# Kernel tuning notes

Measured on AMD Instinct MI355X. Metric: run time of the kernel, lower is better.

## Reference

```python
import jax, jax.numpy as jnp
import numpy as np

SIGMA_S = 10.0
SIGMA_R = 0.5
NUM_ITER = 3
EPS = 1e-8


def _gauss_kernel(sigma_s):
    # static python (sigma_s is config), matches torch code exactly
    ks = min(int(6 * sigma_s + 1), 61)
    if ks % 2 == 0:
        ks -= 1
    hk = ks // 2
    x = jnp.arange(-hk, hk + 1, dtype=jnp.float32)
    g = jnp.exp(-(x ** 2) / (2.0 * sigma_s ** 2))
    return g / g.sum(), hk


def _depthwise_1d(img, g, hk, axis):
    """Depthwise Gaussian conv along axis (2=H, 3=W) with replicate padding.
    img: [B,C,H,W]. Equivalent to the original unfold+gaussian reduction."""
    C = img.shape[1]
    ks = g.shape[0]
    pad = [(0, 0)] * 4
    pad[axis] = (hk, hk)
    p = jnp.pad(img, pad, mode='edge')
    if axis == 3:
        rhs = jnp.broadcast_to(g.reshape(1, 1, 1, ks), (C, 1, 1, ks))
    else:
        rhs = jnp.broadcast_to(g.reshape(1, 1, ks, 1), (C, 1, ks, 1))
    return jax.lax.conv_general_dilated(
        p, rhs, window_strides=(1, 1), padding='VALID',
        dimension_numbers=('NCHW', 'OIHW', 'NCHW'),
        feature_group_count=C)


def _edge_weights(guide, sigma_r):
    # grad along W, replicate last column; grad along H, replicate last row
    gx = guide[:, :, :, 1:] - guide[:, :, :, :-1]
    gx = jnp.pad(gx, ((0, 0), (0, 0), (0, 0), (0, 1)), mode='edge')
    gy = guide[:, :, 1:, :] - guide[:, :, :-1, :]
    gy = jnp.pad(gy, ((0, 0), (0, 0), (0, 1), (0, 0)), mode='edge')
    inv2s2 = 1.0 / (2.0 * sigma_r ** 2)
    wx = jnp.exp(-(gx ** 2) * inv2s2)
    wy = jnp.exp(-(gy ** 2) * inv2s2)
    return wx, wy


def _dt_filter(input_img):
    # guide = channel mean (C>1 branch of the original)
    guide = input_img.mean(axis=1, keepdims=True)  # [B,1,H,W]
    wx, wy = _edge_weights(guide, SIGMA_R)
    # NOTE: in the original, weight = gauss_k * w(x); weight_sum = w(x)*sum(gauss)+eps
    # = w(x)+eps (gauss is normalized). Since w(x) is constant over k, the weighted
    # reduction factorizes exactly: out = (w/(w+eps)) * gaussian_conv(img).
    # Same math, no [B,C,H,W,K] unfold tensor.
    sx = wx / (wx + EPS)  # scale used by vertical filter
    sy = wy / (wy + EPS)  # scale used by horizontal filter
    out = input_img
    for i in range(NUM_ITER):
        sigma_i = SIGMA_S * 2 ** i
        g, hk = _gauss_kernel(sigma_i)
        out = _depthwise_1d(out, g, hk, axis=3) * sy  # horizontal, vert-grad weights
        out = _depthwise_1d(out, g, hk, axis=2) * sx  # vertical, horiz-grad weights
    return out  # mode='denoise': no detail enhancement


def setup_inputs() -> dict:
    key = jax.random.key(0)
    input_img = jax.random.uniform(key, (8, 3, 1024, 1024), dtype=jnp.float32)
    return {"input_img": input_img}


def reference(input_img):
    return _dt_filter(input_img)
```

## Files before the change

kernel.cpp:

```cpp
#include <hip/hip_runtime.h>
#include <math.h>


#define HH 1024
#define WW 1024
#define BB 8
#define CC 3
#define KS 61
#define HK 30

struct GW { float w[KS]; };

__global__ __launch_bounds__(512) void hconv(const float* __restrict__ in,
                                             float* __restrict__ out, GW g) {
    __shared__ float tile[64][193];
    const int xt  = blockIdx.x;
    const int yt  = blockIdx.y;
    const int bc  = blockIdx.z;
    const int tid = threadIdx.x;

    const float* src   = in + (size_t)bc * (HH * (size_t)WW);
    const int    xbase = xt * 128 - 32;
    const int    y0    = yt * 64;

    {
        const int rg = tid >> 6, lane = tid & 63;
        #pragma unroll
        for (int k = 0; k < 8; ++k) {
            const int r = rg + 8 * k;
            const float* srow = src + (size_t)(y0 + r) * WW;
            #pragma unroll
            for (int m = 0; m < 3; ++m) {
                const int c = lane + 64 * m;
                int gx = xbase + c;
                gx = min(max(gx, 0), WW - 1);
                tile[r][c] = srow[gx];
            }
        }
    }
    __syncthreads();

    const int y  = tid & 63;
    const int xg = tid >> 6;
    const int cb = xg * 16 + 2;

    float acc[16];
    #pragma unroll
    for (int i = 0; i < 16; ++i) acc[i] = 0.f;

    #pragma unroll
    for (int j = 0; j < 16 + KS - 1; ++j) {
        const float v = tile[y][cb + j];
        #pragma unroll
        for (int i = 0; i < 16; ++i) {
            const int t = j - i;
            if (t >= 0 && t < KS)
                acc[i] = fmaf(g.w[t], v, acc[i]);
        }
    }

    float* dst = out + (size_t)bc * (HH * (size_t)WW)
                     + (size_t)(y0 + y) * WW + xt * 128 + xg * 16;
    #pragma unroll
    for (int i = 0; i < 4; ++i)
        *(float4*)(dst + 4 * i) = make_float4(acc[4*i], acc[4*i+1],
                                              acc[4*i+2], acc[4*i+3]);
}

__global__ __launch_bounds__(512) void vconv(const float* __restrict__ in,
                                             float* __restrict__ out, GW g) {
    __shared__ float tile[(128 + 2 * HK) * 64];
    const int bx0 = blockIdx.x * 64;
    const int ty0 = blockIdx.y * 128;
    const int bc  = blockIdx.z;
    const int tid = threadIdx.x;

    const float* src = in + (size_t)bc * (HH * (size_t)WW);

    {
        const int rg = tid >> 5, lane = tid & 31;
        #pragma unroll
        for (int k = 0; k < 12; ++k) {
            const int r = rg + 16 * k;
            if (r < 188) {
                int gy = ty0 + r - HK;
                gy = min(max(gy, 0), HH - 1);
                const float2* srow = (const float2*)(src + (size_t)gy * WW + bx0);
                ((float2*)tile)[r * 32 + lane] = srow[lane];
            }
        }
    }
    __syncthreads();

    const int x  = tid & 63;
    const int yg = tid >> 6;
    const int yo = yg * 16;

    float acc[16];
    #pragma unroll
    for (int i = 0; i < 16; ++i) acc[i] = 0.f;

    #pragma unroll
    for (int j = 0; j < 16 + KS - 1; ++j) {
        const float v = tile[(yo + j) * 64 + x];
        #pragma unroll
        for (int i = 0; i < 16; ++i) {
            const int t = j - i;
            if (t >= 0 && t < KS)
                acc[i] = fmaf(g.w[t], v, acc[i]);
        }
    }

    float* dst = out + (size_t)bc * (HH * (size_t)WW)
                     + (size_t)(ty0 + yo) * WW + bx0 + x;
    #pragma unroll
    for (int i = 0; i < 16; ++i) dst[(size_t)i * WW] = acc[i];
}

static void fill_w(double sigma, GW* g) {
    double tmp[KS], s = 0.0;
    for (int k = 0; k < KS; ++k) {
        const double d = (double)(k - HK);
        tmp[k] = exp(-(d * d) / (2.0 * sigma * sigma));
        s += tmp[k];
    }
    for (int k = 0; k < KS; ++k) g->w[k] = (float)(tmp[k] / s);
}

extern "C" void kernel_launch(void* const* d_in, const int* in_sizes, int n_in,
                              void* d_out, int out_size, void* d_ws, size_t ws_size,
                              hipStream_t stream) {
    const float* input = (const float*)d_in[0];
    float* out = (float*)d_out;
    float* tmp = (float*)d_ws;

    GW g10, g20, g40;
    fill_w(10.0, &g10);
    fill_w(20.0, &g20);
    fill_w(40.0, &g40);

    const dim3 hb(512), hg(WW / 128, HH / 64, BB * CC);
    const dim3 vb(512), vg(WW / 64, HH / 128, BB * CC);

    hconv<<<hg, hb, 0, stream>>>(input, tmp, g10);
    vconv<<<vg, vb, 0, stream>>>(tmp, out, g10);
    hconv<<<hg, hb, 0, stream>>>(out, tmp, g20);
    vconv<<<vg, vb, 0, stream>>>(tmp, out, g20);
    hconv<<<hg, hb, 0, stream>>>(out, tmp, g40);
    vconv<<<vg, vb, 0, stream>>>(tmp, out, g40);
}
```

Baseline: 451.9 us.

## Drop shared-memory tiles and register-block 32 outputs per thread in both convolutions

Both the horizontal and vertical Gaussian passes stop staging a tile in LDS and instead read inputs straight from global memory. The horizontal pass uses float4 row loads, with clamping only at image edges. Each thread now accumulates 32 outputs in registers instead of 16, which cuts the halo overhead per output, and the grids are reshaped to match. This removes LDS traffic and the block barrier, in exchange for relying on the L1/L2 caches for overlapping window reads and for higher register pressure, which may lower occupancy.

```diff
diff --git a/kernel.cpp b/kernel.cpp
--- a/kernel.cpp
+++ b/kernel.cpp
@@ -11,110 +11,83 @@
 
 struct GW { float w[KS]; };
 
-__global__ __launch_bounds__(512) void hconv(const float* __restrict__ in,
+__global__ __launch_bounds__(256) void hconv(const float* __restrict__ in,
                                              float* __restrict__ out, GW g) {
-    __shared__ float tile[64][193];
-    const int xt  = blockIdx.x;
-    const int yt  = blockIdx.y;
+    const int tid = threadIdx.x;
+    const int seg = tid & 31;
+    const int row = tid >> 5;
+    const int y   = blockIdx.x * 8 + row;
     const int bc  = blockIdx.z;
-    const int tid = threadIdx.x;
 
-    const float* src   = in + (size_t)bc * (HH * (size_t)WW);
-    const int    xbase = xt * 128 - 32;
-    const int    y0    = yt * 64;
+    const float* __restrict__ srow = in + ((size_t)bc * HH + y) * WW;
+    const int X  = seg * 32;
+    const int xw = X - 32;
 
-    {
-        const int rg = tid >> 6, lane = tid & 63;
+    float acc[32];
+    #pragma unroll
+    for (int i = 0; i < 32; ++i) acc[i] = 0.f;
+
+    #pragma unroll
+    for (int k = 0; k < 24; ++k) {
+        const int gx = xw + 4 * k;
+        float4 v;
+        if (gx >= 0 && gx <= WW - 4) {
+            v = *(const float4*)(srow + gx);
+        } else {
+            const int a0 = min(max(gx    , 0), WW - 1);
+            const int a1 = min(max(gx + 1, 0), WW - 1);
+            const int a2 = min(max(gx + 2, 0), WW - 1);
+            const int a3 = min(max(gx + 3, 0), WW - 1);
+            v = make_float4(srow[a0], srow[a1], srow[a2], srow[a3]);
+        }
+        const float vv[4] = { v.x, v.y, v.z, v.w };
         #pragma unroll
-        for (int k = 0; k < 8; ++k) {
-            const int r = rg + 8 * k;
-            const float* srow = src + (size_t)(y0 + r) * WW;
+        for (int c = 0; c < 4; ++c) {
+            const int j = 4 * k + c;
             #pragma unroll
-            for (int m = 0; m < 3; ++m) {
-                const int c = lane + 64 * m;
-                int gx = xbase + c;
-                gx = min(max(gx, 0), WW - 1);
-                tile[r][c] = srow[gx];
+            for (int i = 0; i < 32; ++i) {
+                const int t = j - 2 - i;
+                if (t >= 0 && t < KS)
+                    acc[i] = fmaf(g.w[t], vv[c], acc[i]);
             }
         }
     }
-    __syncthreads();
 
-    const int y  = tid & 63;
-    const int xg = tid >> 6;
-    const int cb = xg * 16 + 2;
+    float* drow = out + ((size_t)bc * HH + y) * WW + X;
+    #pragma unroll
+    for (int i = 0; i < 8; ++i)
+        *(float4*)(drow + 4 * i) =
+            make_float4(acc[4*i], acc[4*i+1], acc[4*i+2], acc[4*i+3]);
+}
 
-    float acc[16];
+__global__ __launch_bounds__(256) void vconv(const float* __restrict__ in,
+                                             float* __restrict__ out, GW g) {
+    const int x  = blockIdx.x * 256 + threadIdx.x;
+    const int Y  = blockIdx.y * 32;
+    const int bc = blockIdx.z;
+
+    const float* __restrict__ src = in + (size_t)bc * (HH * (size_t)WW);
+
+    float acc[32];
     #pragma unroll
-    for (int i = 0; i < 16; ++i) acc[i] = 0.f;
+    for (int i = 0; i < 32; ++i) acc[i] = 0.f;
 
     #pragma unroll
-    for (int j = 0; j < 16 + KS - 1; ++j) {
-        const float v = tile[y][cb + j];
+    for (int j = 0; j < 32 + KS - 1; ++j) {
+        int gy = Y - HK + j;
+        gy = min(max(gy, 0), HH - 1);
+        const float v = src[(size_t)gy * WW + x];
         #pragma unroll
-        for (int i = 0; i < 16; ++i) {
+        for (int i = 0; i < 32; ++i) {
             const int t = j - i;
             if (t >= 0 && t < KS)
                 acc[i] = fmaf(g.w[t], v, acc[i]);
         }
     }
 
-    float* dst = out + (size_t)bc * (HH * (size_t)WW)
-                     + (size_t)(y0 + y) * WW + xt * 128 + xg * 16;
+    float* dst = out + (size_t)bc * (HH * (size_t)WW) + (size_t)Y * WW + x;
     #pragma unroll
-    for (int i = 0; i < 4; ++i)
-        *(float4*)(dst + 4 * i) = make_float4(acc[4*i], acc[4*i+1],
-                                              acc[4*i+2], acc[4*i+3]);
-}
-
-__global__ __launch_bounds__(512) void vconv(const float* __restrict__ in,
-                                             float* __restrict__ out, GW g) {
-    __shared__ float tile[(128 + 2 * HK) * 64];
-    const int bx0 = blockIdx.x * 64;
-    const int ty0 = blockIdx.y * 128;
-    const int bc  = blockIdx.z;
-    const int tid = threadIdx.x;
-
-    const float* src = in + (size_t)bc * (HH * (size_t)WW);
-
-    {
-        const int rg = tid >> 5, lane = tid & 31;
-        #pragma unroll
-        for (int k = 0; k < 12; ++k) {
-            const int r = rg + 16 * k;
-            if (r < 188) {
-                int gy = ty0 + r - HK;
-                gy = min(max(gy, 0), HH - 1);
-                const float2* srow = (const float2*)(src + (size_t)gy * WW + bx0);
-                ((float2*)tile)[r * 32 + lane] = srow[lane];
-            }
-        }
-    }
-    __syncthreads();
-
-    const int x  = tid & 63;
-    const int yg = tid >> 6;
-    const int yo = yg * 16;
-
-    float acc[16];
-    #pragma unroll
-    for (int i = 0; i < 16; ++i) acc[i] = 0.f;
-
-    #pragma unroll
-    for (int j = 0; j < 16 + KS - 1; ++j) {
-        const float v = tile[(yo + j) * 64 + x];
-        #pragma unroll
-        for (int i = 0; i < 16; ++i) {
-            const int t = j - i;
-            if (t >= 0 && t < KS)
-                acc[i] = fmaf(g.w[t], v, acc[i]);
-        }
-    }
-
-    float* dst = out + (size_t)bc * (HH * (size_t)WW)
-                     + (size_t)(ty0 + yo) * WW + bx0 + x;
-    #pragma unroll
-    for (int i = 0; i < 16; ++i) dst[(size_t)i * WW] = acc[i];
+    for (int i = 0; i < 32; ++i) dst[(size_t)i * WW] = acc[i];
 }
 
 static void fill_w(double sigma, GW* g) {
@@ -139,8 +112,8 @@
     fill_w(20.0, &g20);
     fill_w(40.0, &g40);
 
-    const dim3 hb(512), hg(WW / 128, HH / 64, BB * CC);
-    const dim3 vb(512), vg(WW / 64, HH / 128, BB * CC);
+    const dim3 hb(256), hg(HH / 8, 1, BB * CC);
+    const dim3 vb(256), vg(WW / 256, HH / 32, BB * CC);
 
     hconv<<<hg, hb, 0, stream>>>(input, tmp, g10);
     vconv<<<vg, vb, 0, stream>>>(tmp, out, g10);
```

Measured after the change: 1.555 ms. 244% more time.

## Compose three Gaussian passes into one 181-tap filter with separate edge kernels

Applied to the files above, without the earlier changes.

Precomputes, on the host, the convolution of the sigma 10, 20 and 40 Gaussians into a single 181-tap kernel. Interior pixels are then filtered with one horizontal and one vertical pass instead of three of each. The border bands, where replicate padding breaks that composition, get dedicated kernels that chain the three 61-tap passes inside shared memory. This cuts global memory round trips and launches, at the cost of larger shared tiles, lower occupancy from 256-thread blocks, and extra edge launches.

```diff
diff --git a/kernel.cpp b/kernel.cpp
--- a/kernel.cpp
+++ b/kernel.cpp
@@ -6,125 +6,290 @@
 #define WW 1024
 #define BB 8
 #define CC 3
-#define KS 61
-#define HK 30
-
-struct GW { float w[KS]; };
-
-__global__ __launch_bounds__(512) void hconv(const float* __restrict__ in,
-                                             float* __restrict__ out, GW g) {
-    __shared__ float tile[64][193];
-    const int xt  = blockIdx.x;
-    const int yt  = blockIdx.y;
-    const int bc  = blockIdx.z;
-    const int tid = threadIdx.x;
-
-    const float* src   = in + (size_t)bc * (HH * (size_t)WW);
-    const int    xbase = xt * 128 - 32;
-    const int    y0    = yt * 64;
-
+
+struct GW181 { float w[181]; };
+struct GW3   { float a[61]; float b[61]; float c[61]; };
+
+__global__ __launch_bounds__(256) void hfused(const float* __restrict__ in,
+                                              float* __restrict__ out, GW181 g) {
+    __shared__ float tile[32][309];
+    const int x0 = 90 + 128 * blockIdx.x;
+    const int y0 = blockIdx.y * 32;
+    const int bc = blockIdx.z;
+    const int t  = threadIdx.x;
+
+    const float* __restrict__ src = in + ((size_t)bc * HH + y0) * WW;
     {
-        const int rg = tid >> 6, lane = tid & 63;
+        const int lane = t & 63, rg = t >> 6;
         #pragma unroll
         for (int k = 0; k < 8; ++k) {
+            const int r = rg + 4 * k;
+            const float* srow = src + (size_t)r * WW;
+            #pragma unroll
+            for (int m = 0; m < 5; ++m) {
+                const int c = lane + 64 * m;
+                if (c < 308) tile[r][c] = srow[min(x0 - 90 + c, WW - 1)];
+            }
+        }
+    }
+    __syncthreads();
+
+    const int y = t & 31, xg = t >> 5;
+    float acc[16];
+    #pragma unroll
+    for (int i = 0; i < 16; ++i) acc[i] = 0.f;
+
+    #pragma unroll
+    for (int j = 0; j < 196; ++j) {
+        const float v = tile[y][xg * 16 + j];
+        #pragma unroll
+        for (int i = 0; i < 16; ++i) {
+            const int tt = j - i;
+            if (tt >= 0 && tt < 181) acc[i] = fmaf(g.w[tt], v, acc[i]);
+        }
+    }
+
+    float* drow = out + ((size_t)bc * HH + y0 + y) * WW + x0 + xg * 16;
+    #pragma unroll
+    for (int i = 0; i < 16; ++i)
+        if (x0 + xg * 16 + i < 934) drow[i] = acc[i];
+}
+
+__global__ __launch_bounds__(256) void vfused(const float* __restrict__ in,
+                                              float* __restrict__ out, GW181 g) {
+    __shared__ float tile[308][32];
+    const int Y0 = 90 + 128 * blockIdx.x;
+    const int x0 = blockIdx.y * 32;
+    const int bc = blockIdx.z;
+    const int t  = threadIdx.x;
+
+    const float* __restrict__ src = in + (size_t)bc * (HH * (size_t)WW);
+    {
+        const int col = t & 31, rg = t >> 5;
+        #pragma unroll
+        for (int k = 0; k < 39; ++k) {
             const int r = rg + 8 * k;
-            const float* srow = src + (size_t)(y0 + r) * WW;
-            #pragma unroll
-            for (int m = 0; m < 3; ++m) {
+            if (r < 308) {
+                const int u = min(Y0 - 90 + r, HH - 1);
+                tile[r][col] = src[(size_t)u * WW + x0 + col];
+            }
+        }
+    }
+    __syncthreads();
+
+    const int col = t & 31, yo = (t >> 5) * 16;
+    float acc[16];
+    #pragma unroll
+    for (int i = 0; i < 16; ++i) acc[i] = 0.f;
+
+    #pragma unroll
+    for (int j = 0; j < 196; ++j) {
+        const float v = tile[yo + j][col];
+        #pragma unroll
+        for (int i = 0; i < 16; ++i) {
+            const int tt = j - i;
+            if (tt >= 0 && tt < 181) acc[i] = fmaf(g.w[tt], v, acc[i]);
+        }
+    }
+
+    float* dst = out + (size_t)bc * (HH * (size_t)WW) + x0 + col;
+    #pragma unroll
+    for (int i = 0; i < 16; ++i) {
+        const int yy = Y0 + yo + i;
+        if (yy < 934) dst[(size_t)yy * WW] = acc[i];
+    }
+}
+
+__global__ __launch_bounds__(256) void hedge(const float* __restrict__ in,
+                                             float* __restrict__ out, GW3 g) {
+    __shared__ float s0[16][217], s1[16][185], s2[16][153];
+    const int ys   = blockIdx.x;
+    const int bc   = blockIdx.y;
+    const int side = blockIdx.z;
+    const int t    = threadIdx.x;
+
+    const float* __restrict__ src = in + ((size_t)bc * HH + ys * 16) * WW;
+    {
+        const int lane = t & 63, rg = t >> 6;
+        #pragma unroll
+        for (int k = 0; k < 4; ++k) {
+            const int r = rg + 4 * k;
+            #pragma unroll
+            for (int m = 0; m < 4; ++m) {
                 const int c = lane + 64 * m;
-                int gx = xbase + c;
-                gx = min(max(gx, 0), WW - 1);
-                tile[r][c] = srow[gx];
-            }
-        }
-    }
-    __syncthreads();
-
-    const int y  = tid & 63;
-    const int xg = tid >> 6;
-    const int cb = xg * 16 + 2;
-
-    float acc[16];
-    #pragma unroll
-    for (int i = 0; i < 16; ++i) acc[i] = 0.f;
-
-    #pragma unroll
-    for (int j = 0; j < 16 + KS - 1; ++j) {
-        const float v = tile[y][cb + j];
-        #pragma unroll
-        for (int i = 0; i < 16; ++i) {
-            const int t = j - i;
-            if (t >= 0 && t < KS)
-                acc[i] = fmaf(g.w[t], v, acc[i]);
-        }
-    }
-
-    float* dst = out + (size_t)bc * (HH * (size_t)WW)
-                     + (size_t)(y0 + y) * WW + xt * 128 + xg * 16;
-    #pragma unroll
-    for (int i = 0; i < 4; ++i)
-        *(float4*)(dst + 4 * i) = make_float4(acc[4*i], acc[4*i+1],
-                                              acc[4*i+2], acc[4*i+3]);
-}
-
-__global__ __launch_bounds__(512) void vconv(const float* __restrict__ in,
-                                             float* __restrict__ out, GW g) {
-    __shared__ float tile[(128 + 2 * HK) * 64];
-    const int bx0 = blockIdx.x * 64;
-    const int ty0 = blockIdx.y * 128;
-    const int bc  = blockIdx.z;
-    const int tid = threadIdx.x;
-
-    const float* src = in + (size_t)bc * (HH * (size_t)WW);
-
+                if (c < 217) {
+                    int u = max(c - 32, 0);
+                    if (side) u = WW - 1 - u;
+                    s0[r][c] = src[(size_t)r * WW + u];
+                }
+            }
+        }
+    }
+    __syncthreads();
+
+    const int y = t >> 4, xl = t & 15;
+
+    if (xl < 15) {
+        float a[10];
+        #pragma unroll
+        for (int i = 0; i < 10; ++i) a[i] = 0.f;
+        const int z0 = 10 * xl;
+        #pragma unroll
+        for (int j = 0; j < 70; ++j) {
+            const float v = s0[y][z0 + 2 + j];
+            #pragma unroll
+            for (int i = 0; i < 10; ++i) {
+                const int r = j - i;
+                if (r >= 0 && r < 61) a[i] = fmaf(g.a[r], v, a[i]);
+            }
+        }
+        #pragma unroll
+        for (int i = 0; i < 10; ++i) s1[y][z0 + 32 + i] = a[i];
+        if (xl == 0)
+            for (int p = 0; p < 32; ++p) s1[y][p] = a[0];
+    }
+    __syncthreads();
+
+    if (xl < 15) {
+        float a[8];
+        #pragma unroll
+        for (int i = 0; i < 8; ++i) a[i] = 0.f;
+        const int z0 = 8 * xl;
+        #pragma unroll
+        for (int j = 0; j < 68; ++j) {
+            const float v = s1[y][z0 + 2 + j];
+            #pragma unroll
+            for (int i = 0; i < 8; ++i) {
+                const int r = j - i;
+                if (r >= 0 && r < 61) a[i] = fmaf(g.b[r], v, a[i]);
+            }
+        }
+        #pragma unroll
+        for (int i = 0; i < 8; ++i) s2[y][z0 + 32 + i] = a[i];
+        if (xl == 0)
+            for (int p = 0; p < 32; ++p) s2[y][p] = a[0];
+    }
+    __syncthreads();
+
+    if (xl < 15) {
+        float a[6];
+        #pragma unroll
+        for (int i = 0; i < 6; ++i) a[i] = 0.f;
+        const int z0 = 6 * xl;
+        #pragma unroll
+        for (int j = 0; j < 66; ++j) {
+            const float v = s2[y][z0 + 2 + j];
+            #pragma unroll
+            for (int i = 0; i < 6; ++i) {
+                const int r = j - i;
+                if (r >= 0 && r < 61) a[i] = fmaf(g.c[r], v, a[i]);
+            }
+        }
+        float* drow = out + ((size_t)bc * HH + ys * 16 + y) * WW;
+        #pragma unroll
+        for (int i = 0; i < 6; ++i) {
+            const int gx = z0 + i;
+            drow[side ? (WW - 1 - gx) : gx] = a[i];
+        }
+    }
+}
+
+__global__ __launch_bounds__(256) void vedge(const float* __restrict__ in,
+                                             float* __restrict__ out, GW3 g) {
+    __shared__ float s0[217][17], s1[185][17], s2[153][17];
+    const int xs   = blockIdx.x;
+    const int bc   = blockIdx.y;
+    const int side = blockIdx.z;
+    const int t    = threadIdx.x;
+    const int cx   = t & 15, zl = t >> 4;
+
+    const float* __restrict__ src = in + (size_t)bc * (HH * (size_t)WW);
     {
-        const int rg = tid >> 5, lane = tid & 31;
-        #pragma unroll
-        for (int k = 0; k < 12; ++k) {
-            const int r = rg + 16 * k;
-            if (r < 188) {
-                int gy = ty0 + r - HK;
-                gy = min(max(gy, 0), HH - 1);
-                const float2* srow = (const float2*)(src + (size_t)gy * WW + bx0);
-                ((float2*)tile)[r * 32 + lane] = srow[lane];
-            }
-        }
-    }
-    __syncthreads();
-
-    const int x  = tid & 63;
-    const int yg = tid >> 6;
-    const int yo = yg * 16;
-
-    float acc[16];
-    #pragma unroll
-    for (int i = 0; i < 16; ++i) acc[i] = 0.f;
-
-    #pragma unroll
-    for (int j = 0; j < 16 + KS - 1; ++j) {
-        const float v = tile[(yo + j) * 64 + x];
-        #pragma unroll
-        for (int i = 0; i < 16; ++i) {
-            const int t = j - i;
-            if (t >= 0 && t < KS)
-                acc[i] = fmaf(g.w[t], v, acc[i]);
-        }
-    }
-
-    float* dst = out + (size_t)bc * (HH * (size_t)WW)
-                     + (size_t)(ty0 + yo) * WW + bx0 + x;
-    #pragma unroll
-    for (int i = 0; i < 16; ++i) dst[(size_t)i * WW] = acc[i];
-}
-
-static void fill_w(double sigma, GW* g) {
-    double tmp[KS], s = 0.0;
-    for (int k = 0; k < KS; ++k) {
-        const double d = (double)(k - HK);
-        tmp[k] = exp(-(d * d) / (2.0 * sigma * sigma));
-        s += tmp[k];
-    }
-    for (int k = 0; k < KS; ++k) g->w[k] = (float)(tmp[k] / s);
+        #pragma unroll
+        for (int k = 0; k < 14; ++k) {
+            const int r = zl + 16 * k;
+            if (r < 217) {
+                int u = max(r - 32, 0);
+                if (side) u = HH - 1 - u;
+                s0[r][cx] = src[(size_t)u * WW + xs * 16 + cx];
+            }
+        }
+    }
+    __syncthreads();
+
+    if (zl < 15) {
+        float a[10];
+        #pragma unroll
+        for (int i = 0; i < 10; ++i) a[i] = 0.f;
+        const int z0 = 10 * zl;
+        #pragma unroll
+        for (int j = 0; j < 70; ++j) {
+            const float v = s0[z0 + 2 + j][cx];
+            #pragma unroll
+            for (int i = 0; i < 10; ++i) {
+                const int r = j - i;
+                if (r >= 0 && r < 61) a[i] = fmaf(g.a[r], v, a[i]);
+            }
+        }
+        #pragma unroll
+        for (int i = 0; i < 10; ++i) s1[z0 + 32 + i][cx] = a[i];
+        if (zl == 0)
+            for (int p = 0; p < 32; ++p) s1[p][cx] = a[0];
+    }
+    __syncthreads();
+
+    if (zl < 15) {
+        float a[8];
+        #pragma unroll
+        for (int i = 0; i < 8; ++i) a[i] = 0.f;
+        const int z0 = 8 * zl;
+        #pragma unroll
+        for (int j = 0; j < 68; ++j) {
+            const float v = s1[z0 + 2 + j][cx];
+            #pragma unroll
+            for (int i = 0; i < 8; ++i) {
+                const int r = j - i;
+                if (r >= 0 && r < 61) a[i] = fmaf(g.b[r], v, a[i]);
+            }
+        }
+        #pragma unroll
+        for (int i = 0; i < 8; ++i) s2[z0 + 32 + i][cx] = a[i];
+        if (zl == 0)
+            for (int p = 0; p < 32; ++p) s2[p][cx] = a[0];
+    }
+    __syncthreads();
+
+    if (zl < 15) {
+        float a[6];
+        #pragma unroll
+        for (int i = 0; i < 6; ++i) a[i] = 0.f;
+        const int z0 = 6 * zl;
+        #pragma unroll
+        for (int j = 0; j < 66; ++j) {
+            const float v = s2[z0 + 2 + j][cx];
+            #pragma unroll
+            for (int i = 0; i < 6; ++i) {
+                const int r = j - i;
+                if (r >= 0 && r < 61) a[i] = fmaf(g.c[r], v, a[i]);
+            }
+        }
+        #pragma unroll
+        for (int i = 0; i < 6; ++i) {
+            const int gy = z0 + i;
+            const int Y  = side ? (HH - 1 - gy) : gy;
+            out[(size_t)bc * (HH * (size_t)WW) + (size_t)Y * WW + xs * 16 + cx] = a[i];
+        }
+    }
+}
+
+static void gauss61(double sigma, double* w) {
+    double s = 0.0;
+    for (int k = 0; k < 61; ++k) {
+        const double d = (double)(k - 30);
+        w[k] = exp(-(d * d) / (2.0 * sigma * sigma));
+        s += w[k];
+    }
+    for (int k = 0; k < 61; ++k) w[k] /= s;
 }
 
 extern "C" void kernel_launch(void* const* d_in, const int* in_sizes, int n_in,
@@ -134,18 +299,32 @@
     float* out = (float*)d_out;
     float* tmp = (float*)d_ws;
 
-    GW g10, g20, g40;
-    fill_w(10.0, &g10);
-    fill_w(20.0, &g20);
-    fill_w(40.0, &g40);
-
-    const dim3 hb(512), hg(WW / 128, HH / 64, BB * CC);
-    const dim3 vb(512), vg(WW / 64, HH / 128, BB * CC);
-
-    hconv<<<hg, hb, 0, stream>>>(input, tmp, g10);
-    vconv<<<vg, vb, 0, stream>>>(tmp, out, g10);
-    hconv<<<hg, hb, 0, stream>>>(out, tmp, g20);
-    vconv<<<vg, vb, 0, stream>>>(tmp, out, g20);
-    hconv<<<hg, hb, 0, stream>>>(out, tmp, g40);
-    vconv<<<vg, vb, 0, stream>>>(tmp, out, g40);
-}
+    double w10[61], w20[61], w40[61], c1[121], W[181];
+    gauss61(10.0, w10); gauss61(20.0, w20); gauss61(40.0, w40);
+    for (int k = 0; k < 121; ++k) c1[k] = 0.0;
+    for (int i = 0; i < 61; ++i)
+        for (int j = 0; j < 61; ++j) c1[i + j] += w10[i] * w20[j];
+    for (int k = 0; k < 181; ++k) W[k] = 0.0;
+    for (int i = 0; i < 121; ++i)
+        for (int j = 0; j < 61; ++j) W[i + j] += c1[i] * w40[j];
+
+    GW181 gi;
+    for (int k = 0; k < 181; ++k) gi.w[k] = (float)W[k];
+    GW3 ge;
+    for (int k = 0; k < 61; ++k) {
+        ge.a[k] = (float)w10[k];
+        ge.b[k] = (float)w20[k];
+        ge.c[k] = (float)w40[k];
+    }
+
+    const dim3 tb(256);
+    const dim3 gh(7, 32, BB * CC);
+    const dim3 gv(7, 32, BB * CC);
+    const dim3 ge_h(64, BB * CC, 2);
+    const dim3 ge_v(64, BB * CC, 2);
+
+    hfused<<<gh, tb, 0, stream>>>(input, tmp, gi);
+    hedge <<<ge_h, tb, 0, stream>>>(input, tmp, ge);
+    vfused<<<gv, tb, 0, stream>>>(tmp, out, gi);
+    vedge <<<ge_v, tb, 0, stream>>>(tmp, out, ge);
+}
```

Measured after the change: 766.3 us. 1.7x slower.
